# Optimization experiments

Measured on AMD Instinct MI355X. Metric: run time of the kernel, lower is better.

Reference implementation:

```python
import jax, jax.numpy as jnp
import numpy as np

C_IN = 256
C_OUT = 256


def setup_inputs() -> dict:
    key = jax.random.key(0)
    k1, k2, k3, k4, k5 = jax.random.split(key, 5)
    B, C, H, W = 4, C_IN, 64, 64
    x = jax.random.normal(k1, (B, C, H, W), dtype=jnp.float32)
    y = jax.random.normal(k2, (B, C, H, W), dtype=jnp.float32)
    s = 1.0 / np.sqrt(C_IN)  # kaiming-ish init scale for 1x1 conv
    wq = jax.random.normal(k3, (C_OUT, C_IN), dtype=jnp.float32) * s
    wk = jax.random.normal(k4, (C_OUT, C_IN), dtype=jnp.float32) * s
    wv = jax.random.normal(k5, (C_OUT, C_IN), dtype=jnp.float32) * s
    gamma = jnp.ones((1,), dtype=jnp.float32) * 0.1
    return {"x": x, "y": y, "wq": wq, "wk": wk, "wv": wv, "gamma": gamma}


def reference(x, y, wq, wk, wv, gamma):
    B, C, H, W = x.shape
    N = H * W
    xf = x.reshape(B, C, N)  # [B, C, N]
    yf = y.reshape(B, C, N)
    q = jnp.einsum('oc,bcn->bno', wq, xf)   # [B, N, Co]
    k = jnp.einsum('oc,bcn->bon', wk, yf)   # [B, Co, N]
    v = jnp.einsum('oc,bcn->bon', wv, yf)   # [B, Co, N]
    energy = jnp.einsum('bio,boj->bij', q, k)          # [B, N, N]
    attention = jax.nn.softmax(energy, axis=-1)
    out = jnp.einsum('bcj,bij->bci', v, attention)     # [B, Co, N]
    out = out.reshape(B, -1, H, W)
    return gamma[0] * out + x
```

## Files before the change

### kernel.cpp

```cpp
#include <hip/hip_runtime.h>
#include <hip/hip_bf16.h>
#include <stdint.h>

#define C_DIM 256
#define N_DIM 4096
#define B_DIM 4

typedef __attribute__((ext_vector_type(8))) short s16x8;
typedef __attribute__((ext_vector_type(4))) short s16x4;
typedef __attribute__((ext_vector_type(4))) float f32x4;
typedef __attribute__((ext_vector_type(16))) float f32x16;
typedef __attribute__((ext_vector_type(4))) int i32x4;

static __device__ __forceinline__ short f2bs(float f) {
    __bf16 h = (__bf16)f;
    return __builtin_bit_cast(short, h);
}
static __device__ __forceinline__ float bs2f(short s) {
    unsigned int u = ((unsigned int)(unsigned short)s) << 16;
    return __builtin_bit_cast(float, u);
}
static __device__ __forceinline__ unsigned cvtpk(float lo, float hi) {
    unsigned r;
    asm("v_cvt_pk_bf16_f32 %0, %1, %2" : "=v"(r) : "v"(lo), "v"(hi));
    return r;
}
static __device__ __forceinline__ void plswap(unsigned &a, unsigned &b) {
    asm("v_permlane32_swap_b32 %0, %1" : "+v"(a), "+v"(b));
}

__global__ __launch_bounds__(256)
void proj_kernel(const float* __restrict__ x, const float* __restrict__ y,
                 const float* __restrict__ wq, const float* __restrict__ wk,
                 const float* __restrict__ wv,
                 short* __restrict__ Qb, short* __restrict__ Kb,
                 short* __restrict__ Vb)
{
    int bid = blockIdx.x;
    int nt = bid & 63;
    int b  = (bid >> 6) & 3;
    int p  = bid >> 8;
    int n0 = nt * 64;
    const float* src = (p == 0) ? x : y;
    const float* w   = (p == 0) ? wq : (p == 1) ? wk : wv;

    __shared__ __align__(16) short Xs[64][264];
    __shared__ __align__(16) short Ws[64][264];
    __shared__ short T[64][66];

    int t = threadIdx.x;
    int l = t & 63;
    int wv_ = t >> 6;

    for (int ct = 0; ct < 4; ++ct) {
        #pragma unroll
        for (int pp = 0; pp < 16; ++pp) {
            int c = wv_ + pp * 4;
            float v = src[((size_t)(b * C_DIM + ct * 64 + c)) * N_DIM + n0 + l];
            T[l][c] = f2bs(v);
        }
        __syncthreads();
        #pragma unroll
        for (int pp = 0; pp < 16; ++pp) {
            int n = wv_ + pp * 4;
            Xs[n][ct * 64 + l] = T[n][l];
        }
        __syncthreads();
    }

    int lane = t & 63;
    int wid = t >> 6;
    int m = lane & 15, q = lane >> 4;

    for (int ot = 0; ot < 4; ++ot) {
        int o0 = ot * 64;
        #pragma unroll
        for (int pas = 0; pas < 8; ++pas) {
            int slot = pas * 256 + t;
            int row = slot >> 5, ck = slot & 31;
            const float* wr = &w[(size_t)(o0 + row) * C_DIM + ck * 8];
            f32x4 a  = *(const f32x4*)wr;
            f32x4 b4 = *(const f32x4*)(wr + 4);
            s16x8 r;
            r[0]=f2bs(a[0]);  r[1]=f2bs(a[1]);  r[2]=f2bs(a[2]);  r[3]=f2bs(a[3]);
            r[4]=f2bs(b4[0]); r[5]=f2bs(b4[1]); r[6]=f2bs(b4[2]); r[7]=f2bs(b4[3]);
            *(s16x8*)&Ws[row][ck * 8] = r;
        }
        __syncthreads();

        f32x4 acc[4] = {};
        if (p < 2) {
            #pragma unroll
            for (int kk = 0; kk < 8; ++kk) {
                s16x8 af = *(const s16x8*)&Xs[wid * 16 + m][kk * 32 + q * 8];
                #pragma unroll
                for (int ob = 0; ob < 4; ++ob) {
                    s16x8 bf = *(const s16x8*)&Ws[ob * 16 + m][kk * 32 + q * 8];
                    acc[ob] = __builtin_amdgcn_mfma_f32_16x16x32_bf16(af, bf, acc[ob], 0, 0, 0);
                }
            }
            float sc = (p == 0) ? 1.4426950408889634f : 1.0f;
            short* dst = ((p == 0) ? Qb : Kb) + (size_t)b * N_DIM * C_DIM;
            #pragma unroll
            for (int ob = 0; ob < 4; ++ob)
                #pragma unroll
                for (int r = 0; r < 4; ++r) {
                    int n = n0 + wid * 16 + q * 4 + r;
                    int o = o0 + ob * 16 + m;
                    dst[(size_t)n * C_DIM + o] = f2bs(acc[ob][r] * sc);
                }
        } else {
            #pragma unroll
            for (int kk = 0; kk < 8; ++kk) {
                s16x8 af = *(const s16x8*)&Ws[wid * 16 + m][kk * 32 + q * 8];
                #pragma unroll
                for (int nb = 0; nb < 4; ++nb) {
                    s16x8 bf = *(const s16x8*)&Xs[nb * 16 + m][kk * 32 + q * 8];
                    acc[nb] = __builtin_amdgcn_mfma_f32_16x16x32_bf16(af, bf, acc[nb], 0, 0, 0);
                }
            }
            short* dst = Vb + (size_t)b * C_DIM * N_DIM;
            #pragma unroll
            for (int nb = 0; nb < 4; ++nb)
                #pragma unroll
                for (int r = 0; r < 4; ++r) {
                    int o = o0 + wid * 16 + q * 4 + r;
                    int n = n0 + nb * 16 + m;
                    dst[(size_t)o * N_DIM + n] = f2bs(acc[nb][r]);
                }
        }
        __syncthreads();
    }
}

__global__ __launch_bounds__(256, 2)
void attn_kernel(const short* __restrict__ Qb, const short* __restrict__ Kb,
                 const short* __restrict__ Vb,
                 short* __restrict__ Op01, short* __restrict__ Op23,
                 float* __restrict__ ms)
{
    int bid0 = blockIdx.x;
    int swz = (bid0 & 7) * 64 + (bid0 >> 3);
    int b  = swz >> 7;
    int ks = (swz >> 5) & 3;
    int qt = swz & 31;
    int i0 = qt * 128;

    int t = threadIdx.x;
    int wv = t >> 6;
    int lane = t & 63;
    int il = lane & 31, hi = lane >> 5;
    int q0 = i0 + wv * 32;

    __shared__ __align__(16) short Ksh[32][264];
    __shared__ __align__(16) short Vsh[256][40];

    const short* Qp = Qb + (size_t)b * N_DIM * C_DIM;
    const short* Kp = Kb + (size_t)b * N_DIM * C_DIM + (size_t)(ks * 1024) * C_DIM;
    const short* Vp = Vb + (size_t)b * C_DIM * N_DIM + ks * 1024;

    s16x8 qf[16];
    {
        const short* qrow = Qp + (size_t)(q0 + il) * C_DIM + hi * 8;
        #pragma unroll
        for (int kk = 0; kk < 16; ++kk)
            qf[kk] = *(const s16x8*)&qrow[kk * 16];
    }

    int krb = t >> 5, kck = t & 31;
    int vrb = t >> 2, vck = t & 3;

    {
        s16x8 kr[4], vr[4];
        #pragma unroll
        for (int p = 0; p < 4; ++p)
            kr[p] = *(const s16x8*)&Kp[(size_t)(p * 8 + krb) * C_DIM + kck * 8];
        #pragma unroll
        for (int p = 0; p < 4; ++p)
            vr[p] = *(const s16x8*)&Vp[(size_t)(p * 64 + vrb) * N_DIM + vck * 8];
        #pragma unroll
        for (int p = 0; p < 4; ++p) *(s16x8*)&Ksh[p * 8 + krb][kck * 8] = kr[p];
        #pragma unroll
        for (int p = 0; p < 4; ++p) *(s16x8*)&Vsh[p * 64 + vrb][vck * 8] = vr[p];
    }
    __syncthreads();

    f32x16 acc[8] = {};
    float srun = 0.f;

    for (int jt = 0; jt < 32; ++jt) {
        bool pfch = (jt < 31);

        f32x16 sv0 = {}, sv1 = {};
        __builtin_amdgcn_s_setprio(1);
        #pragma unroll
        for (int kk = 0; kk < 8; ++kk) {
            s16x8 a0 = *(const s16x8*)&Ksh[il][kk * 16 + hi * 8];
            sv0 = __builtin_amdgcn_mfma_f32_32x32x16_bf16(a0, qf[kk], sv0, 0, 0, 0);
            s16x8 a1 = *(const s16x8*)&Ksh[il][(kk + 8) * 16 + hi * 8];
            sv1 = __builtin_amdgcn_mfma_f32_32x32x16_bf16(a1, qf[kk + 8], sv1, 0, 0, 0);
        }
        __builtin_amdgcn_s_setprio(0);

        s16x8 kr[4];
        if (pfch) {
            const short* kg = Kp + (size_t)((jt + 1) * 32) * C_DIM;
            #pragma unroll
            for (int p = 0; p < 4; ++p)
                kr[p] = *(const s16x8*)&kg[(size_t)(p * 8 + krb) * C_DIM + kck * 8];
        }

        #pragma unroll
        for (int r = 0; r < 16; ++r) {
            float pe = exp2f((sv0[r] + sv1[r]) - 64.f);
            sv0[r] = pe;
            srun += pe;
        }

        unsigned d0[4], d1[4];
        #pragma unroll
        for (int rq = 0; rq < 4; ++rq) {
            d0[rq] = cvtpk(sv0[4 * rq + 0], sv0[4 * rq + 1]);
            d1[rq] = cvtpk(sv0[4 * rq + 2], sv0[4 * rq + 3]);
        }
        unsigned w0a = d0[0], w2a = d0[1]; plswap(w0a, w2a);
        unsigned w1a = d1[0], w3a = d1[1]; plswap(w1a, w3a);
        unsigned w0b = d0[2], w2b = d0[3]; plswap(w0b, w2b);
        unsigned w1b = d1[2], w3b = d1[3]; plswap(w1b, w3b);
        i32x4 pi0 = { (int)w0a, (int)w1a, (int)w2a, (int)w3a };
        i32x4 pi1 = { (int)w0b, (int)w1b, (int)w2b, (int)w3b };
        s16x8 pf0 = __builtin_bit_cast(s16x8, pi0);
        s16x8 pf1 = __builtin_bit_cast(s16x8, pi1);

        s16x8 vr[4];
        if (pfch) {
            const short* vg = Vp + (jt + 1) * 32;
            #pragma unroll
            for (int p = 0; p < 4; ++p)
                vr[p] = *(const s16x8*)&vg[(size_t)(p * 64 + vrb) * N_DIM + vck * 8];
        }

        __builtin_amdgcn_s_setprio(1);
        #pragma unroll
        for (int cs = 0; cs < 8; ++cs) {
            s16x8 va = *(const s16x8*)&Vsh[cs * 32 + il][hi * 8];
            acc[cs] = __builtin_amdgcn_mfma_f32_32x32x16_bf16(va, pf0, acc[cs], 0, 0, 0);
            s16x8 vb = *(const s16x8*)&Vsh[cs * 32 + il][16 + hi * 8];
            acc[cs] = __builtin_amdgcn_mfma_f32_32x32x16_bf16(vb, pf1, acc[cs], 0, 0, 0);
        }
        __builtin_amdgcn_s_setprio(0);

        __syncthreads();
        if (pfch) {
            #pragma unroll
            for (int p = 0; p < 4; ++p) *(s16x8*)&Ksh[p * 8 + krb][kck * 8] = kr[p];
            #pragma unroll
            for (int p = 0; p < 4; ++p) *(s16x8*)&Vsh[p * 64 + vrb][vck * 8] = vr[p];
        }
        __syncthreads();
    }

    srun += __shfl_xor(srun, 32, 64);
    int i = q0 + il;
    const size_t HSZ = (size_t)B_DIM * C_DIM * N_DIM;
    if (ks < 2) {
        short* o = Op01 + (size_t)ks * HSZ + (size_t)(b * C_DIM) * N_DIM + i;
        #pragma unroll
        for (int cs = 0; cs < 8; ++cs)
            #pragma unroll
            for (int r = 0; r < 16; ++r) {
                int c = cs * 32 + (r & 3) + 8 * (r >> 2) + 4 * hi;
                o[(size_t)c * N_DIM] = f2bs(acc[cs][r]);
            }
    } else {
        short* o = Op23 + ((size_t)(b * C_DIM) * N_DIM + i) * 2 + (ks - 2);
        #pragma unroll
        for (int cs = 0; cs < 8; ++cs)
            #pragma unroll
            for (int r = 0; r < 16; ++r) {
                int c = cs * 32 + (r & 3) + 8 * (r >> 2) + 4 * hi;
                o[(size_t)c * N_DIM * 2] = f2bs(acc[cs][r]);
            }
    }
    if (hi == 0) {
        float* msp = ms + (size_t)(ks * B_DIM + b) * N_DIM;
        msp[i] = srun;
    }
}

__global__ __launch_bounds__(256)
void merge_kernel(const short* __restrict__ Op01, const short* Op23,
                  const float* __restrict__ ms, const float* __restrict__ x,
                  const float* __restrict__ gamma, float* out)
{
    size_t base = ((size_t)blockIdx.x * 256 + threadIdx.x) * 8;
    int n = (int)(base & (N_DIM - 1));
    int b = (int)(base >> 20);
    const size_t HSZ = (size_t)B_DIM * C_DIM * N_DIM;

    s16x8 o0 = *(const s16x8*)&Op01[base];
    s16x8 o1 = *(const s16x8*)&Op01[HSZ + base];
    s16x8 pa = *(const s16x8*)&Op23[base * 2];
    s16x8 pb = *(const s16x8*)&Op23[base * 2 + 8];

    f32x4 den[2] = {};
    #pragma unroll
    for (int h = 0; h < 4; ++h) {
        const float* msp = ms + (size_t)(h * B_DIM + b) * N_DIM + n;
        f32x4 sa = *(const f32x4*)&msp[0];
        f32x4 sb = *(const f32x4*)&msp[4];
        #pragma unroll
        for (int e = 0; e < 4; ++e) { den[0][e] += sa[e]; den[1][e] += sb[e]; }
    }
    f32x4 xa = *(const f32x4*)&x[base];
    f32x4 xb = *(const f32x4*)&x[base + 4];
    float g = gamma[0];

    float res[8];
    #pragma unroll
    for (int e = 0; e < 8; ++e) {
        int half = e >> 2, e4 = e & 3;
        float o2 = bs2f(e < 4 ? pa[2 * e]     : pb[2 * (e - 4)]);
        float o3 = bs2f(e < 4 ? pa[2 * e + 1] : pb[2 * (e - 4) + 1]);
        float num = bs2f(o0[e]) + bs2f(o1[e]) + o2 + o3;
        float xv = (e < 4) ? xa[e4] : xb[e4];
        res[e] = g * (num / den[half][e4]) + xv;
    }
    f32x4 ra = { res[0], res[1], res[2], res[3] };
    f32x4 rb = { res[4], res[5], res[6], res[7] };
    *(f32x4*)&out[base] = ra;
    *(f32x4*)&out[base + 4] = rb;
}

extern "C" void kernel_launch(void* const* d_in, const int* in_sizes, int n_in,
                              void* d_out, int out_size, void* d_ws, size_t ws_size,
                              hipStream_t stream) {
    const float* x  = (const float*)d_in[0];
    const float* y  = (const float*)d_in[1];
    const float* wq = (const float*)d_in[2];
    const float* wk = (const float*)d_in[3];
    const float* wv = (const float*)d_in[4];
    const float* gm = (const float*)d_in[5];
    float* out = (float*)d_out;

    char* ws = (char*)d_ws;
    const size_t SZ = (size_t)B_DIM * N_DIM * C_DIM * sizeof(short);
    short* Qb = (short*)(ws + 2 * SZ);
    short* Kb = (short*)(ws + 3 * SZ);
    short* Vb = (short*)(ws + 4 * SZ);
    short* Op01 = (short*)ws;
    float* ms = (float*)(ws + 5 * SZ);

    proj_kernel<<<dim3(768), dim3(256), 0, stream>>>(x, y, wq, wk, wv, Qb, Kb, Vb);
    attn_kernel<<<dim3(512), dim3(256), 0, stream>>>(Qb, Kb, Vb, Op01, (short*)out, ms);
    merge_kernel<<<dim3(2048), dim3(256), 0, stream>>>(Op01, (const short*)out, ms, x, gm, out);
}
```

Baseline: 125.4 us.

## Double-buffer K/V tiles with direct global-to-LDS K loads and XOR swizzle

The attention kernel now keeps two LDS buffers for the K and V tiles. K is loaded straight into the next buffer with global_load_lds and an XOR swizzle in place of row padding, which avoids bank conflicts. V is stored into the next buffer mid-iteration, so one of the two barriers per iteration is removed and loads overlap compute. LDS use roughly doubles, which may affect the two-blocks-per-CU occupancy target, and the asynchronous LDS writes depend on correct wait handling at the barrier.

```diff
diff --git a/kernel.cpp b/kernel.cpp
--- a/kernel.cpp
+++ b/kernel.cpp
@@ -27,6 +27,11 @@
 }
 static __device__ __forceinline__ void plswap(unsigned &a, unsigned &b) {
     asm("v_permlane32_swap_b32 %0, %1" : "+v"(a), "+v"(b));
+}
+static __device__ __forceinline__ void g2l16(const short* g, short* l) {
+    __builtin_amdgcn_global_load_lds(
+        (const __attribute__((address_space(1))) unsigned int*)g,
+        (__attribute__((address_space(3))) unsigned int*)l, 16, 0, 0);
 }
 
 __global__ __launch_bounds__(256)
@@ -151,9 +156,10 @@
     int lane = t & 63;
     int il = lane & 31, hi = lane >> 5;
     int q0 = i0 + wv * 32;
-
-    __shared__ __align__(16) short Ksh[32][264];
-    __shared__ __align__(16) short Vsh[256][40];
+    int xsw = il & 7;
+
+    __shared__ __align__(16) short Ksh[2][32][256];
+    __shared__ __align__(16) short Vsh[2][256][40];
 
     const short* Qp = Qb + (size_t)b * N_DIM * C_DIM;
     const short* Kp = Kb + (size_t)b * N_DIM * C_DIM + (size_t)(ks * 1024) * C_DIM;
@@ -167,21 +173,21 @@
             qf[kk] = *(const s16x8*)&qrow[kk * 16];
     }
 
-    int krb = t >> 5, kck = t & 31;
     int vrb = t >> 2, vck = t & 3;
 
     {
-        s16x8 kr[4], vr[4];
-        #pragma unroll
-        for (int p = 0; p < 4; ++p)
-            kr[p] = *(const s16x8*)&Kp[(size_t)(p * 8 + krb) * C_DIM + kck * 8];
+        #pragma unroll
+        for (int p = 0; p < 4; ++p) {
+            int r = (wv * 4 + p) * 2 + (lane >> 5);
+            int gs = (lane & 31) ^ (r & 7);
+            g2l16(Kp + (size_t)r * C_DIM + gs * 8, &Ksh[0][(wv * 4 + p) * 2][0]);
+        }
+        s16x8 vr[4];
         #pragma unroll
         for (int p = 0; p < 4; ++p)
             vr[p] = *(const s16x8*)&Vp[(size_t)(p * 64 + vrb) * N_DIM + vck * 8];
         #pragma unroll
-        for (int p = 0; p < 4; ++p) *(s16x8*)&Ksh[p * 8 + krb][kck * 8] = kr[p];
-        #pragma unroll
-        for (int p = 0; p < 4; ++p) *(s16x8*)&Vsh[p * 64 + vrb][vck * 8] = vr[p];
+        for (int p = 0; p < 4; ++p) *(s16x8*)&Vsh[0][p * 64 + vrb][vck * 8] = vr[p];
     }
     __syncthreads();
 
@@ -190,24 +196,35 @@
 
     for (int jt = 0; jt < 32; ++jt) {
         bool pfch = (jt < 31);
+        int cur = jt & 1, nx = cur ^ 1;
+
+        if (pfch) {
+            const short* kg = Kp + (size_t)((jt + 1) * 32) * C_DIM;
+            #pragma unroll
+            for (int p = 0; p < 4; ++p) {
+                int r = (wv * 4 + p) * 2 + (lane >> 5);
+                int gs = (lane & 31) ^ (r & 7);
+                g2l16(kg + (size_t)r * C_DIM + gs * 8, &Ksh[nx][(wv * 4 + p) * 2][0]);
+            }
+        }
 
         f32x16 sv0 = {}, sv1 = {};
         __builtin_amdgcn_s_setprio(1);
         #pragma unroll
         for (int kk = 0; kk < 8; ++kk) {
-            s16x8 a0 = *(const s16x8*)&Ksh[il][kk * 16 + hi * 8];
+            s16x8 a0 = *(const s16x8*)&Ksh[cur][il][((kk * 2 + hi) ^ xsw) * 8];
             sv0 = __builtin_amdgcn_mfma_f32_32x32x16_bf16(a0, qf[kk], sv0, 0, 0, 0);
-            s16x8 a1 = *(const s16x8*)&Ksh[il][(kk + 8) * 16 + hi * 8];
+            s16x8 a1 = *(const s16x8*)&Ksh[cur][il][(((kk + 8) * 2 + hi) ^ xsw) * 8];
             sv1 = __builtin_amdgcn_mfma_f32_32x32x16_bf16(a1, qf[kk + 8], sv1, 0, 0, 0);
         }
         __builtin_amdgcn_s_setprio(0);
 
-        s16x8 kr[4];
+        s16x8 vr[4];
         if (pfch) {
-            const short* kg = Kp + (size_t)((jt + 1) * 32) * C_DIM;
+            const short* vg = Vp + (jt + 1) * 32;
             #pragma unroll
             for (int p = 0; p < 4; ++p)
-                kr[p] = *(const s16x8*)&kg[(size_t)(p * 8 + krb) * C_DIM + kck * 8];
+                vr[p] = *(const s16x8*)&vg[(size_t)(p * 64 + vrb) * N_DIM + vck * 8];
         }
 
         #pragma unroll
@@ -232,31 +249,22 @@
         s16x8 pf0 = __builtin_bit_cast(s16x8, pi0);
         s16x8 pf1 = __builtin_bit_cast(s16x8, pi1);
 
-        s16x8 vr[4];
         if (pfch) {
-            const short* vg = Vp + (jt + 1) * 32;
             #pragma unroll
             for (int p = 0; p < 4; ++p)
-                vr[p] = *(const s16x8*)&vg[(size_t)(p * 64 + vrb) * N_DIM + vck * 8];
+                *(s16x8*)&Vsh[nx][p * 64 + vrb][vck * 8] = vr[p];
         }
 
         __builtin_amdgcn_s_setprio(1);
         #pragma unroll
         for (int cs = 0; cs < 8; ++cs) {
-            s16x8 va = *(const s16x8*)&Vsh[cs * 32 + il][hi * 8];
+            s16x8 va = *(const s16x8*)&Vsh[cur][cs * 32 + il][hi * 8];
             acc[cs] = __builtin_amdgcn_mfma_f32_32x32x16_bf16(va, pf0, acc[cs], 0, 0, 0);
-            s16x8 vb = *(const s16x8*)&Vsh[cs * 32 + il][16 + hi * 8];
+            s16x8 vb = *(const s16x8*)&Vsh[cur][cs * 32 + il][16 + hi * 8];
             acc[cs] = __builtin_amdgcn_mfma_f32_32x32x16_bf16(vb, pf1, acc[cs], 0, 0, 0);
         }
         __builtin_amdgcn_s_setprio(0);
 
-        __syncthreads();
-        if (pfch) {
-            #pragma unroll
-            for (int p = 0; p < 4; ++p) *(s16x8*)&Ksh[p * 8 + krb][kck * 8] = kr[p];
-            #pragma unroll
-            for (int p = 0; p < 4; ++p) *(s16x8*)&Vsh[p * 64 + vrb][vck * 8] = vr[p];
-        }
         __syncthreads();
     }
 
```

Measured after the change: 150.7 us. 20.2% more time.
